# Kernel optimization log

Hardware: AMD Instinct MI355X
Metric: run time of the kernel (lower is better)

## Reference

```python
import jax, jax.numpy as jnp
import numpy as np

B, T, C, H, D = 4, 1024, 1024, 16, 64  # batch, seq, n_embd, heads, head_size


def setup_inputs() -> dict:
    key = jax.random.key(0)
    ks = jax.random.split(key, 6)
    x = jax.random.normal(ks[0], (B, T, C), dtype=jnp.float32)
    s = 0.02
    Wq = jax.random.normal(ks[1], (H, C, D), dtype=jnp.float32) * s
    Wk = jax.random.normal(ks[2], (H, C, D), dtype=jnp.float32) * s
    Wv = jax.random.normal(ks[3], (H, C, D), dtype=jnp.float32) * s
    Wo = jax.random.normal(ks[4], (H * D, C), dtype=jnp.float32) * s
    bo = jnp.zeros((C,), dtype=jnp.float32)
    return {"x": x, "Wq": Wq, "Wk": Wk, "Wv": Wv, "Wo": Wo, "bo": bo}


def reference(x, Wq, Wk, Wv, Wo, bo):
    # per-head projections (bias=False Linears), all heads batched via einsum
    q = jnp.einsum("btc,hcd->bhtd", x, Wq)
    k = jnp.einsum("btc,hcd->bhtd", x, Wk)
    v = jnp.einsum("btc,hcd->bhtd", x, Wv)
    # scaled dot-product scores: [B,H,T,T]
    scale = 1.0 / jnp.sqrt(jnp.asarray(D, dtype=q.dtype))
    scores = jnp.einsum("bhtd,bhsd->bhts", q, k) * scale
    # causal mask (tril), masked_fill with -inf equivalent
    causal = jnp.tril(jnp.ones((T, T), dtype=bool))
    neg = jnp.finfo(scores.dtype).min
    scores = jnp.where(causal[None, None], scores, neg)
    att = jax.nn.softmax(scores, axis=-1)
    # weighted aggregation of values, then concat heads
    out = jnp.einsum("bhts,bhsd->bhtd", att, v)
    out = out.transpose(0, 2, 1, 3).reshape(B, T, H * D)
    # output projection
    return out @ Wo + bo
```

## Files before the change

kernel.cpp:

```cpp
#include <hip/hip_runtime.h>
#include <hip/hip_bf16.h>
#include <stdint.h>


typedef float f32x4 __attribute__((ext_vector_type(4)));
typedef __bf16 bf16x8 __attribute__((ext_vector_type(8)));
typedef __bf16 bf16x4 __attribute__((ext_vector_type(4)));

#define GAS __attribute__((address_space(1)))
#define LAS __attribute__((address_space(3)))

__global__ __launch_bounds__(256) void cast_bf16_kernel(
    const float* __restrict__ in, __bf16* __restrict__ out, int n4) {
  int i = blockIdx.x * 256 + threadIdx.x;
  if (i < n4) {
    float4 f = ((const float4*)in)[i];
    bf16x4 o;
    o[0] = (__bf16)f.x; o[1] = (__bf16)f.y; o[2] = (__bf16)f.z; o[3] = (__bf16)f.w;
    ((bf16x4*)out)[i] = o;
  }
}

__global__ __launch_bounds__(256) void transpose_qkv_kernel(
    const float* __restrict__ Wq, const float* __restrict__ Wk,
    const float* __restrict__ Wv, __bf16* __restrict__ dst_base) {
  __shared__ float tile[64][65];
  int z = blockIdx.z;
  const float* s = (z < 16 ? Wq : (z < 32 ? Wk : Wv)) + (size_t)(z & 15) * 65536;
  __bf16* d = dst_base + (size_t)z * 65536;
  int r0 = blockIdx.x * 64;
  int tx = threadIdx.x & 63, ty = threadIdx.x >> 6;
#pragma unroll
  for (int rr = ty; rr < 64; rr += 4)
    tile[rr][tx] = s[(size_t)(r0 + rr) * 64 + tx];
  __syncthreads();
#pragma unroll
  for (int rr = ty; rr < 64; rr += 4)
    d[(size_t)rr * 1024 + (r0 + tx)] = (__bf16)tile[tx][rr];
}

__global__ __launch_bounds__(256) void transpose_cast_kernel(
    const float* __restrict__ src, __bf16* __restrict__ dst,
    int src_ld, int dst_ld) {
  __shared__ float tile[64][65];
  int r0 = blockIdx.x * 64, c0 = blockIdx.y * 64;
  int tx = threadIdx.x & 63, ty = threadIdx.x >> 6;
#pragma unroll
  for (int rr = ty; rr < 64; rr += 4)
    tile[rr][tx] = src[(size_t)(r0 + rr) * src_ld + (c0 + tx)];
  __syncthreads();
#pragma unroll
  for (int rr = ty; rr < 64; rr += 4)
    dst[(size_t)(c0 + rr) * dst_ld + (r0 + tx)] = (__bf16)tile[tx][rr];
}

template <int MODE>
__global__ __launch_bounds__(256) void gemm_bt_kernel(
    const __bf16* __restrict__ A, const __bf16* __restrict__ BT, int N,
    __bf16* __restrict__ qo, __bf16* __restrict__ ko, __bf16* __restrict__ vo,
    float* __restrict__ Cout, const float* __restrict__ bias) {
  constexpr int K = 1024;
  extern __shared__ __align__(16) char smem_raw[];
  __bf16* Ash = (__bf16*)smem_raw;
  __bf16* Bsh = Ash + 2 * 128 * 64;
  const int tid = threadIdx.x;
  const int wid = tid >> 6, lane = tid & 63;
  const int fr = lane & 15, fq = lane >> 4;
  const int m0 = blockIdx.x * 128, n0 = blockIdx.y * 128;
  const int wr = wid >> 1, wc = wid & 1;
  const int lrow8 = lane >> 3;
  const int sc = ((lane & 7) ^ lrow8) * 8;

  f32x4 acc[4][4] = {};

  auto stage = [&](int k0, int buf) {
#pragma unroll
    for (int j = 0; j < 4; ++j) {
      int cc = j * 4 + wid;
      int row = cc * 8 + lrow8;
      const __bf16* gA = A + (size_t)(m0 + row) * K + k0 + sc;
      const __bf16* gB = BT + (size_t)(n0 + row) * K + k0 + sc;
      __builtin_amdgcn_global_load_lds((const GAS void*)gA, (LAS void*)&Ash[buf * 8192 + cc * 512], 16, 0, 0);
      __builtin_amdgcn_global_load_lds((const GAS void*)gB, (LAS void*)&Bsh[buf * 8192 + cc * 512], 16, 0, 0);
    }
  };

  stage(0, 0);
  __syncthreads();
  int buf = 0;
  for (int k0 = 0; k0 < K; k0 += 64) {
    if (k0 + 64 < K) stage(k0 + 64, buf ^ 1);
#pragma unroll
    for (int kk = 0; kk < 2; ++kk) {
      const int ch = ((((kk << 2) | fq)) ^ (fr & 7)) * 8;
      bf16x8 af[4], bfr[4];
#pragma unroll
      for (int mi = 0; mi < 4; ++mi) {
        int r = wr * 64 + mi * 16 + fr;
        af[mi] = *(const bf16x8*)&Ash[buf * 8192 + r * 64 + ch];
      }
#pragma unroll
      for (int ni = 0; ni < 4; ++ni) {
        int r = wc * 64 + ni * 16 + fr;
        bfr[ni] = *(const bf16x8*)&Bsh[buf * 8192 + r * 64 + ch];
      }
      __builtin_amdgcn_s_setprio(1);
#pragma unroll
      for (int mi = 0; mi < 4; ++mi)
#pragma unroll
        for (int ni = 0; ni < 4; ++ni)
          acc[mi][ni] = __builtin_amdgcn_mfma_f32_16x16x32_bf16(af[mi], bfr[ni], acc[mi][ni], 0, 0, 0);
      __builtin_amdgcn_s_setprio(0);
    }
    __syncthreads();
    buf ^= 1;
  }

  if (MODE == 0 && (n0 >> 10) == 2) {
    __bf16* spill = (__bf16*)smem_raw;
#pragma unroll
    for (int mi = 0; mi < 4; ++mi)
#pragma unroll
      for (int ni = 0; ni < 4; ++ni) {
        int nl = wc * 64 + ni * 16 + fr;
        int ml = wr * 64 + mi * 16 + fq * 4;
        bf16x4 pk;
#pragma unroll
        for (int r = 0; r < 4; ++r) pk[r] = (__bf16)acc[mi][ni][r];
        *(bf16x4*)&spill[nl * 136 + ml] = pk;
      }
    __syncthreads();
    const int b = m0 >> 10, t0 = m0 & 1023;
    const int lrow = lane >> 4, lch = lane & 15;
#pragma unroll
    for (int i = 0; i < 8; ++i) {
      int nl = wid * 32 + i * 4 + lrow;
      bf16x8 v = *(const bf16x8*)&spill[nl * 136 + lch * 8];
      int nn = (n0 & 1023) + nl;
      *(bf16x8*)&vo[(((size_t)b * 16 + (nn >> 6)) * 64 + (nn & 63)) * 1024 + t0 + lch * 8] = v;
    }
    return;
  }

#pragma unroll
  for (int mi = 0; mi < 4; ++mi) {
#pragma unroll
    for (int ni = 0; ni < 4; ++ni) {
      int n = n0 + wc * 64 + ni * 16 + fr;
      int mb = m0 + wr * 64 + mi * 16 + fq * 4;
#pragma unroll
      for (int r = 0; r < 4; ++r) {
        int m = mb + r;
        float val = acc[mi][ni][r];
        if (MODE == 0) {
          int nl = n & 1023;
          int h = nl >> 6, dd = nl & 63;
          int b = m >> 10, t = m & 1023;
          if ((n >> 10) == 0) {
            qo[(((size_t)b * 16 + h) * 1024 + t) * 64 + dd] = (__bf16)(val * 0.125f);
          } else {
            ko[(((size_t)b * 16 + h) * 1024 + t) * 64 + dd] = (__bf16)val;
          }
        } else {
          Cout[(size_t)m * N + n] = val + bias[n];
        }
      }
    }
  }
}

__global__ __launch_bounds__(256) void attn_fwd_kernel(
    const __bf16* __restrict__ Q, const __bf16* __restrict__ Kg,
    const __bf16* __restrict__ Vt, __bf16* __restrict__ O) {
  __shared__ __align__(16) __bf16 Ksh[2][64 * 64];
  __shared__ __align__(16) __bf16 VTs[2][64 * 64];
  __shared__ __align__(16) __bf16 Psh[4][16 * 72];

  const int bid = blockIdx.x;
  const int qt = 15 - (bid >> 6);
  const int bh = bid & 63;
  const int b = bh >> 4, h = bh & 15;
  const size_t base = (size_t)bh * 1024 * 64;
  const int tid = threadIdx.x, wid = tid >> 6, lane = tid & 63;
  const int fr = lane & 15, fq = lane >> 4;
  const int q0 = qt * 64;

  bf16x8 qf[2];
  {
    int qr = q0 + wid * 16 + fr;
    qf[0] = *(const bf16x8*)&Q[base + (size_t)qr * 64 + fq * 8];
    qf[1] = *(const bf16x8*)&Q[base + (size_t)qr * 64 + 32 + fq * 8];
  }
  f32x4 oacc[4] = {};
  float m = -1e30f, l = 0.f;

  const int lrow8 = lane >> 3;
  const int schunk = (lane & 7) ^ lrow8;

  auto stage = [&](int st, int buf) {
    const int s0 = st * 64;
#pragma unroll
    for (int i = 0; i < 2; ++i) {
      int rowbase = i * 32 + wid * 8;
      int row = rowbase + lrow8;
      const __bf16* gK = Kg + base + (size_t)(s0 + row) * 64 + schunk * 8;
      __builtin_amdgcn_global_load_lds((const GAS void*)gK,
          (LAS void*)&Ksh[buf][rowbase * 64], 16, 0, 0);
      const __bf16* gV = Vt + base + (size_t)row * 1024 + s0 + schunk * 8;
      __builtin_amdgcn_global_load_lds((const GAS void*)gV,
          (LAS void*)&VTs[buf][rowbase * 64], 16, 0, 0);
    }
  };

  auto compute = [&](int buf, int s0, bool maskT) {
    f32x4 s[4];
    __builtin_amdgcn_s_setprio(1);
#pragma unroll
    for (int sf = 0; sf < 4; ++sf) {
      int row = sf * 16 + fr, rx = fr & 7;
      bf16x8 kf0 = *(const bf16x8*)&Ksh[buf][row * 64 + ((fq ^ rx) << 3)];
      f32x4 z = {};
      s[sf] = __builtin_amdgcn_mfma_f32_16x16x32_bf16(kf0, qf[0], z, 0, 0, 0);
      bf16x8 kf1 = *(const bf16x8*)&Ksh[buf][row * 64 + (((4 + fq) ^ rx) << 3)];
      s[sf] = __builtin_amdgcn_mfma_f32_16x16x32_bf16(kf1, qf[1], s[sf], 0, 0, 0);
    }
    __builtin_amdgcn_s_setprio(0);

    const int qg = q0 + wid * 16 + fr;
    float sv[4][4];
    float mx = -1e30f;
#pragma unroll
    for (int sf = 0; sf < 4; ++sf)
#pragma unroll
      for (int r = 0; r < 4; ++r) {
        float x = s[sf][r];
        if (maskT) { int sg = s0 + sf * 16 + fq * 4 + r; if (sg > qg) x = -1e30f; }
        sv[sf][r] = x;
        mx = fmaxf(mx, x);
      }
    mx = fmaxf(mx, __shfl_xor(mx, 16));
    mx = fmaxf(mx, __shfl_xor(mx, 32));
    if (__any(mx - m > 8.0f)) {
      float mnew = fmaxf(m, mx);
      float alpha = __expf(m - mnew);
      m = mnew;
      l *= alpha;
      float ar[4];
#pragma unroll
      for (int r = 0; r < 4; ++r) ar[r] = __shfl(alpha, (lane & 48) | (fq * 4 + r));
#pragma unroll
      for (int df = 0; df < 4; ++df)
#pragma unroll
        for (int r = 0; r < 4; ++r) oacc[df][r] *= ar[r];
    }
    float rs = 0.f;
#pragma unroll
    for (int sf = 0; sf < 4; ++sf) {
      bf16x4 pk;
#pragma unroll
      for (int r = 0; r < 4; ++r) {
        float p = __expf(sv[sf][r] - m);
        rs += p;
        pk[r] = (__bf16)p;
      }
      *(bf16x4*)&Psh[wid][fr * 72 + sf * 16 + fq * 4] = pk;
    }
    rs += __shfl_xor(rs, 16);
    rs += __shfl_xor(rs, 32);
    l += rs;

    __builtin_amdgcn_s_setprio(1);
#pragma unroll
    for (int kk = 0; kk < 2; ++kk) {
      bf16x8 pf = *(const bf16x8*)&Psh[wid][fr * 72 + kk * 32 + fq * 8];
#pragma unroll
      for (int df = 0; df < 4; ++df) {
        int row = df * 16 + fr;
        bf16x8 vf = *(const bf16x8*)&VTs[buf][row * 64 + ((((kk << 2) | fq) ^ (fr & 7)) << 3)];
        oacc[df] = __builtin_amdgcn_mfma_f32_16x16x32_bf16(pf, vf, oacc[df], 0, 0, 0);
      }
    }
    __builtin_amdgcn_s_setprio(0);
  };

  stage(0, 0);
  __syncthreads();
  int cur = 0;
  for (int st = 0; st <= qt; ++st) {
    if (st < qt) stage(st + 1, cur ^ 1);
    compute(cur, st * 64, st == qt);
    __syncthreads();
    cur ^= 1;
  }

  float lr[4];
#pragma unroll
  for (int r = 0; r < 4; ++r) lr[r] = __shfl(l, (lane & 48) | (fq * 4 + r));
#pragma unroll
  for (int r = 0; r < 4; ++r) {
    float inv = 1.0f / lr[r];
    int t = q0 + wid * 16 + fq * 4 + r;
    size_t orow = ((size_t)b * 1024 + t) * 1024 + h * 64;
#pragma unroll
    for (int df = 0; df < 4; ++df)
      O[orow + df * 16 + fr] = (__bf16)(oacc[df][r] * inv);
  }
}

extern "C" void kernel_launch(void* const* d_in, const int* in_sizes, int n_in,
                              void* d_out, int out_size, void* d_ws, size_t ws_size,
                              hipStream_t stream) {
  const float* x  = (const float*)d_in[0];
  const float* Wq = (const float*)d_in[1];
  const float* Wk = (const float*)d_in[2];
  const float* Wv = (const float*)d_in[3];
  const float* Wo = (const float*)d_in[4];
  const float* bo = (const float*)d_in[5];
  float* out = (float*)d_out;

  __bf16* xb    = (__bf16*)d_ws;
  __bf16* wqkvT = xb + (size_t)4096 * 1024;
  __bf16* woT   = wqkvT + (size_t)3072 * 1024;
  __bf16* qb    = woT + (size_t)1024 * 1024;
  __bf16* kb    = qb + (size_t)4 * 16 * 1024 * 64;
  __bf16* vtb   = kb + (size_t)4 * 16 * 1024 * 64;
  __bf16* Ob    = vtb + (size_t)4 * 16 * 1024 * 64;

  cast_bf16_kernel<<<4096, 256, 0, stream>>>(x, xb, 4194304 / 4);
  transpose_qkv_kernel<<<dim3(16, 1, 48), 256, 0, stream>>>(Wq, Wk, Wv, wqkvT);
  transpose_cast_kernel<<<dim3(16, 16), 256, 0, stream>>>(Wo, woT, 1024, 1024);

  gemm_bt_kernel<0><<<dim3(32, 24), 256, 65536, stream>>>(xb, wqkvT, 3072, qb, kb, vtb, nullptr, nullptr);

  attn_fwd_kernel<<<1024, 256, 0, stream>>>(qb, kb, vtb, Ob);

  gemm_bt_kernel<1><<<dim3(32, 8), 256, 65536, stream>>>(Ob, woT, 1024,
      nullptr, nullptr, nullptr, out, bo);
}
```

Baseline: 89.93 us.

## Process two query tiles per attention block to reuse staged K/V tiles

Each attention workgroup now handles two 64-row query tiles (rows qs*128.. and +64) instead of one, so every K and V tile staged into LDS is consumed by both query sets. This halves the grid to 512 blocks and cuts global K/V traffic and the number of staging barriers per query row. In exchange each thread keeps two sets of accumulators and softmax state, which raises register pressure, and fewer blocks may leave CUs underfilled or unbalanced under the causal workload.

```diff
diff --git a/kernel.cpp b/kernel.cpp
--- a/kernel.cpp
+++ b/kernel.cpp
@@ -177,22 +177,23 @@
   __shared__ __align__(16) __bf16 Psh[4][16 * 72];
 
   const int bid = blockIdx.x;
-  const int qt = 15 - (bid >> 6);
+  const int qs = 7 - (bid >> 6);
   const int bh = bid & 63;
   const int b = bh >> 4, h = bh & 15;
   const size_t base = (size_t)bh * 1024 * 64;
   const int tid = threadIdx.x, wid = tid >> 6, lane = tid & 63;
   const int fr = lane & 15, fq = lane >> 4;
-  const int q0 = qt * 64;
-
-  bf16x8 qf[2];
-  {
-    int qr = q0 + wid * 16 + fr;
-    qf[0] = *(const bf16x8*)&Q[base + (size_t)qr * 64 + fq * 8];
-    qf[1] = *(const bf16x8*)&Q[base + (size_t)qr * 64 + 32 + fq * 8];
-  }
-  f32x4 oacc[4] = {};
-  float m = -1e30f, l = 0.f;
+  const int qr0 = qs * 128 + wid * 16 + fr;
+  const int qr1 = qr0 + 64;
+
+  bf16x8 qf0[2], qf1[2];
+  qf0[0] = *(const bf16x8*)&Q[base + (size_t)qr0 * 64 + fq * 8];
+  qf0[1] = *(const bf16x8*)&Q[base + (size_t)qr0 * 64 + 32 + fq * 8];
+  qf1[0] = *(const bf16x8*)&Q[base + (size_t)qr1 * 64 + fq * 8];
+  qf1[1] = *(const bf16x8*)&Q[base + (size_t)qr1 * 64 + 32 + fq * 8];
+
+  f32x4 oa0[4] = {}, oa1[4] = {};
+  float m0 = -1e30f, l0 = 0.f, m1 = -1e30f, l1 = 0.f;
 
   const int lrow8 = lane >> 3;
   const int schunk = (lane & 7) ^ lrow8;
@@ -212,7 +213,8 @@
     }
   };
 
-  auto compute = [&](int buf, int s0, bool maskT) {
+  auto compute = [&](int buf, int s0, const bf16x8* qf, f32x4* oacc,
+                     float& m, float& l, int qg, bool maskT) {
     f32x4 s[4];
     __builtin_amdgcn_s_setprio(1);
 #pragma unroll
@@ -226,7 +228,6 @@
     }
     __builtin_amdgcn_s_setprio(0);
 
-    const int qg = q0 + wid * 16 + fr;
     float sv[4][4];
     float mx = -1e30f;
 #pragma unroll
@@ -283,28 +284,34 @@
     __builtin_amdgcn_s_setprio(0);
   };
 
+  const int nst = 2 * qs + 2;
   stage(0, 0);
   __syncthreads();
   int cur = 0;
-  for (int st = 0; st <= qt; ++st) {
-    if (st < qt) stage(st + 1, cur ^ 1);
-    compute(cur, st * 64, st == qt);
+  for (int st = 0; st < nst; ++st) {
+    if (st + 1 < nst) stage(st + 1, cur ^ 1);
+    if (st <= 2 * qs) compute(cur, st * 64, qf0, oa0, m0, l0, qr0, st == 2 * qs);
+    compute(cur, st * 64, qf1, oa1, m1, l1, qr1, st == nst - 1);
     __syncthreads();
     cur ^= 1;
   }
 
-  float lr[4];
-#pragma unroll
-  for (int r = 0; r < 4; ++r) lr[r] = __shfl(l, (lane & 48) | (fq * 4 + r));
-#pragma unroll
-  for (int r = 0; r < 4; ++r) {
-    float inv = 1.0f / lr[r];
-    int t = q0 + wid * 16 + fq * 4 + r;
-    size_t orow = ((size_t)b * 1024 + t) * 1024 + h * 64;
-#pragma unroll
-    for (int df = 0; df < 4; ++df)
-      O[orow + df * 16 + fr] = (__bf16)(oacc[df][r] * inv);
-  }
+  auto epi = [&](const f32x4* oacc, float l, int tbase) {
+    float lr[4];
+#pragma unroll
+    for (int r = 0; r < 4; ++r) lr[r] = __shfl(l, (lane & 48) | (fq * 4 + r));
+#pragma unroll
+    for (int r = 0; r < 4; ++r) {
+      float inv = 1.0f / lr[r];
+      int t = tbase + fq * 4 + r;
+      size_t orow = ((size_t)b * 1024 + t) * 1024 + h * 64;
+#pragma unroll
+      for (int df = 0; df < 4; ++df)
+        O[orow + df * 16 + fr] = (__bf16)(oacc[df][r] * inv);
+    }
+  };
+  epi(oa0, l0, qs * 128 + wid * 16);
+  epi(oa1, l1, qs * 128 + wid * 16 + 64);
 }
 
 extern "C" void kernel_launch(void* const* d_in, const int* in_sizes, int n_in,
@@ -332,7 +339,7 @@
 
   gemm_bt_kernel<0><<<dim3(32, 24), 256, 65536, stream>>>(xb, wqkvT, 3072, qb, kb, vtb, nullptr, nullptr);
 
-  attn_fwd_kernel<<<1024, 256, 0, stream>>>(qb, kb, vtb, Ob);
+  attn_fwd_kernel<<<512, 256, 0, stream>>>(qb, kb, vtb, Ob);
 
   gemm_bt_kernel<1><<<dim3(32, 8), 256, 65536, stream>>>(Ob, woT, 1024,
       nullptr, nullptr, nullptr, out, bo);
```

After: 105.4 us. +17.2%, slower.
